# Optimization experiments

Measured on AMD Instinct MI355X. Metric: run time of the kernel, lower is better.

## Reference

```python
import jax, jax.numpy as jnp
import numpy as np

N_NODES = 50000
N_EDGES = 600000
D = 128
R = 8
EPS = 1e-5


def layer_norm(x, g, b):
    mu = jnp.mean(x, axis=-1, keepdims=True)
    var = jnp.mean(jnp.square(x - mu), axis=-1, keepdims=True)
    return (x - mu) * jax.lax.rsqrt(var + EPS) * g + b


def rgcn(x, src, dst, edge_attr, W, root, bias, num_nodes):
    # x: [N, d], W: [R, d, f], edge_attr: [E, R] soft relation weights
    E = src.shape[0]
    f = W.shape[-1]
    msg = jnp.zeros((E, f), dtype=x.dtype)
    for r in range(W.shape[0]):  # small fixed relation count
        hr = x @ W[r]                       # [N, f]
        msg = msg + hr[src] * edge_attr[:, r][:, None]  # gather + weight
    agg = jax.ops.segment_sum(msg, dst, num_segments=num_nodes)  # scatter-add
    return agg + x @ root + bias


def setup_inputs() -> dict:
    key = jax.random.key(0)
    ks = jax.random.split(key, 12)
    s = 1.0 / np.sqrt(D)
    return {
        "x": jax.random.normal(ks[0], (N_NODES, D), dtype=jnp.float32),
        "edge_index": jax.random.randint(ks[1], (2, N_EDGES), 0, N_NODES, dtype=jnp.int64),
        "edge_attr": jax.random.uniform(ks[2], (N_EDGES, R), dtype=jnp.float32),
        "ln1_g": jnp.ones((D,), jnp.float32),
        "ln1_b": jnp.zeros((D,), jnp.float32),
        "W1": jax.random.normal(ks[3], (R, D, D), jnp.float32) * s,
        "root1": jax.random.normal(ks[4], (D, D), jnp.float32) * s,
        "b1": jnp.zeros((D,), jnp.float32),
        "ln2_g": jnp.ones((D,), jnp.float32),
        "ln2_b": jnp.zeros((D,), jnp.float32),
        "W2": jax.random.normal(ks[5], (R, D, D), jnp.float32) * s,
        "root2": jax.random.normal(ks[6], (D, D), jnp.float32) * s,
        "b2": jnp.zeros((D,), jnp.float32),
    }


def reference(x, edge_index, edge_attr, ln1_g, ln1_b, W1, root1, b1,
              ln2_g, ln2_b, W2, root2, b2):
    src, dst = edge_index[0], edge_index[1]
    identity = x
    out = jax.nn.gelu(layer_norm(x, ln1_g, ln1_b), approximate=False)
    out = rgcn(out, src, dst, edge_attr, W1, root1, b1, x.shape[0])
    out = jax.nn.gelu(layer_norm(out, ln2_g, ln2_b), approximate=False)
    out = rgcn(out, src, dst, edge_attr, W2, root2, b2, x.shape[0])
    return out + identity
```

## Files before the change

### kernel.cpp

```cpp
#include <hip/hip_runtime.h>
#include <hip/hip_bf16.h>

typedef __attribute__((ext_vector_type(8))) short short8;
typedef __attribute__((ext_vector_type(4))) float f32x4;

__device__ __forceinline__ float bf2f(unsigned short u) {
    union { unsigned int i; float f; } v; v.i = ((unsigned int)u) << 16; return v.f;
}
__device__ __forceinline__ unsigned short f2bf(float f) {
    __hip_bfloat16 h = __float2bfloat16(f);
    union { __hip_bfloat16 h; unsigned short u; } v; v.h = h; return v.u;
}
__device__ __forceinline__ float gelu_exact(float t) {
    return 0.5f * t * (1.0f + erff(t * 0.70710678118654752f));
}
__device__ __forceinline__ short8 ntload8(const unsigned short* p) {
    return __builtin_nontemporal_load((const short8*)p);
}

__global__ void prep_w(const float* __restrict__ W1, const float* __restrict__ root1,
                       unsigned short* __restrict__ Bf1,
                       const float* __restrict__ W2, const float* __restrict__ root2,
                       unsigned short* __restrict__ Bf2) {
    int i = blockIdx.x * 256 + threadIdx.x;
    const float* W = W1; const float* root = root1; unsigned short* Bfrag = Bf1;
    if (i >= 1152 * 128) {
        i -= 1152 * 128; W = W2; root = root2; Bfrag = Bf2;
        if (i >= 1152 * 128) return;
    }
    int kp = i >> 7, n = i & 127;
    float v;
    if (kp < 1024) {
        int d = kp >> 3, r = kp & 7;
        v = W[((size_t)r * 128 + d) * 128 + n];
    } else {
        v = root[(size_t)(kp - 1024) * 128 + n];
    }
    int kb = kp >> 5;
    int lane = (((kp >> 3) & 3) << 4) | (n & 15);
    int j = kp & 7;
    int t = n >> 4;
    Bfrag[(((size_t)(kb * 8 + t) * 64 + lane) << 3) + j] = f2bf(v);
}

__global__ void zero_i32(int* __restrict__ p, int n) {
    int i = blockIdx.x * 256 + threadIdx.x;
    if (i < n) p[i] = 0;
}

__global__ void hist_dst(const int* __restrict__ ei, int* __restrict__ cnt, int E) {
    int e = blockIdx.x * 256 + threadIdx.x;
    if (e >= E) return;
    atomicAdd(&cnt[ei[E + e]], 1);
}

__global__ void scan1(const int* __restrict__ cnt, int* __restrict__ part,
                      int* __restrict__ bsum, int N) {
    int i = blockIdx.x * 256 + threadIdx.x;
    int v = (i < N) ? cnt[i] : 0;
    int lane = threadIdx.x & 63, wid = threadIdx.x >> 6;
    int s = v;
    #pragma unroll
    for (int off = 1; off < 64; off <<= 1) {
        int t = __shfl_up(s, off);
        if (lane >= off) s += t;
    }
    __shared__ int wsum[4];
    if (lane == 63) wsum[wid] = s;
    __syncthreads();
    int add = 0;
    for (int w = 0; w < wid; ++w) add += wsum[w];
    s += add;
    part[i] = s - v;
    if (threadIdx.x == 255) bsum[blockIdx.x] = s;
}

__global__ void scan2(int* __restrict__ bsum, int nb) {
    int i = threadIdx.x;
    int v = (i < nb) ? bsum[i] : 0;
    int lane = threadIdx.x & 63, wid = threadIdx.x >> 6;
    int s = v;
    #pragma unroll
    for (int off = 1; off < 64; off <<= 1) {
        int t = __shfl_up(s, off);
        if (lane >= off) s += t;
    }
    __shared__ int wsum[4];
    if (lane == 63) wsum[wid] = s;
    __syncthreads();
    int add = 0;
    for (int w = 0; w < wid; ++w) add += wsum[w];
    s += add;
    if (i < nb) bsum[i] = s - v;
}

__global__ void scan3(const int* __restrict__ part, const int* __restrict__ bsum,
                      int* __restrict__ rowptr, int* __restrict__ woff, int N) {
    int i = blockIdx.x * 256 + threadIdx.x;
    if (i >= N) return;
    int v = part[i] + bsum[blockIdx.x];
    rowptr[i] = v;
    woff[i] = v;
}

__global__ void scatter_edges(const int* __restrict__ ei, const float4* __restrict__ attr,
                              int* __restrict__ woff, int* __restrict__ esrc,
                              float4* __restrict__ eattr, int E) {
    int e = blockIdx.x * 256 + threadIdx.x;
    if (e >= E) return;
    int src = ei[e], dst = ei[E + e];
    int p = atomicAdd(&woff[dst], 1);
    esrc[p] = src;
    eattr[2 * p]     = attr[2 * e];
    eattr[2 * p + 1] = attr[2 * e + 1];
}

__global__ void ln_gelu(const float* __restrict__ x, const float* __restrict__ g,
                        const float* __restrict__ b, unsigned short* __restrict__ y, int N) {
    int row = (blockIdx.x * blockDim.x + threadIdx.x) >> 6;
    if (row >= N) return;
    int lane = threadIdx.x & 63;
    size_t off = (size_t)row * 128 + lane * 2;
    float2 v = *(const float2*)(x + off);
    float s = v.x + v.y;
    #pragma unroll
    for (int o = 32; o; o >>= 1) s += __shfl_xor(s, o);
    float mu = s * (1.0f / 128.0f);
    float d0 = v.x - mu, d1 = v.y - mu;
    float q = d0 * d0 + d1 * d1;
    #pragma unroll
    for (int o = 32; o; o >>= 1) q += __shfl_xor(q, o);
    float rs = rsqrtf(q * (1.0f / 128.0f) + 1e-5f);
    float2 gg = *(const float2*)(g + lane * 2);
    float2 bb = *(const float2*)(b + lane * 2);
    ushort2 o2;
    o2.x = f2bf(gelu_exact(d0 * rs * gg.x + bb.x));
    o2.y = f2bf(gelu_exact(d1 * rs * gg.y + bb.y));
    *(ushort2*)(y + off) = o2;
}

__global__ __launch_bounds__(256) void edge_z(const int* __restrict__ rowptr,
                                              const int* __restrict__ esrc,
                                              const float4* __restrict__ eattr,
                                              const unsigned short* __restrict__ y,
                                              unsigned short* __restrict__ z, int N, int E) {
    int row = (blockIdx.x << 2) + (threadIdx.x >> 6);
    if (row >= N) return;
    int lane = threadIdx.x & 63;
    int e0 = rowptr[row];
    int e1 = (row + 1 < N) ? rowptr[row + 1] : E;
    float a0[8] = {0,0,0,0,0,0,0,0};
    float a1[8] = {0,0,0,0,0,0,0,0};

    const unsigned short* yl = y + lane * 2;

    int e = e0;
    for (; e + 4 <= e1; e += 4) {
        int s0 = esrc[e], s1 = esrc[e + 1], s2 = esrc[e + 2], s3 = esrc[e + 3];
        float4 wA0 = eattr[2 * e],     wA1 = eattr[2 * e + 1];
        float4 wB0 = eattr[2 * e + 2], wB1 = eattr[2 * e + 3];
        float4 wC0 = eattr[2 * e + 4], wC1 = eattr[2 * e + 5];
        float4 wD0 = eattr[2 * e + 6], wD1 = eattr[2 * e + 7];
        unsigned int h0 = *(const unsigned int*)(yl + (size_t)s0 * 128);
        unsigned int h1 = *(const unsigned int*)(yl + (size_t)s1 * 128);
        unsigned int h2 = *(const unsigned int*)(yl + (size_t)s2 * 128);
        unsigned int h3 = *(const unsigned int*)(yl + (size_t)s3 * 128);
        float y00 = bf2f((unsigned short)(h0 & 0xffffu)), y01 = bf2f((unsigned short)(h0 >> 16));
        float y10 = bf2f((unsigned short)(h1 & 0xffffu)), y11 = bf2f((unsigned short)(h1 >> 16));
        float y20 = bf2f((unsigned short)(h2 & 0xffffu)), y21 = bf2f((unsigned short)(h2 >> 16));
        float y30 = bf2f((unsigned short)(h3 & 0xffffu)), y31 = bf2f((unsigned short)(h3 >> 16));
        a0[0] += wA0.x * y00; a1[0] += wA0.x * y01;
        a0[1] += wA0.y * y00; a1[1] += wA0.y * y01;
        a0[2] += wA0.z * y00; a1[2] += wA0.z * y01;
        a0[3] += wA0.w * y00; a1[3] += wA0.w * y01;
        a0[4] += wA1.x * y00; a1[4] += wA1.x * y01;
        a0[5] += wA1.y * y00; a1[5] += wA1.y * y01;
        a0[6] += wA1.z * y00; a1[6] += wA1.z * y01;
        a0[7] += wA1.w * y00; a1[7] += wA1.w * y01;
        a0[0] += wB0.x * y10; a1[0] += wB0.x * y11;
        a0[1] += wB0.y * y10; a1[1] += wB0.y * y11;
        a0[2] += wB0.z * y10; a1[2] += wB0.z * y11;
        a0[3] += wB0.w * y10; a1[3] += wB0.w * y11;
        a0[4] += wB1.x * y10; a1[4] += wB1.x * y11;
        a0[5] += wB1.y * y10; a1[5] += wB1.y * y11;
        a0[6] += wB1.z * y10; a1[6] += wB1.z * y11;
        a0[7] += wB1.w * y10; a1[7] += wB1.w * y11;
        a0[0] += wC0.x * y20; a1[0] += wC0.x * y21;
        a0[1] += wC0.y * y20; a1[1] += wC0.y * y21;
        a0[2] += wC0.z * y20; a1[2] += wC0.z * y21;
        a0[3] += wC0.w * y20; a1[3] += wC0.w * y21;
        a0[4] += wC1.x * y20; a1[4] += wC1.x * y21;
        a0[5] += wC1.y * y20; a1[5] += wC1.y * y21;
        a0[6] += wC1.z * y20; a1[6] += wC1.z * y21;
        a0[7] += wC1.w * y20; a1[7] += wC1.w * y21;
        a0[0] += wD0.x * y30; a1[0] += wD0.x * y31;
        a0[1] += wD0.y * y30; a1[1] += wD0.y * y31;
        a0[2] += wD0.z * y30; a1[2] += wD0.z * y31;
        a0[3] += wD0.w * y30; a1[3] += wD0.w * y31;
        a0[4] += wD1.x * y30; a1[4] += wD1.x * y31;
        a0[5] += wD1.y * y30; a1[5] += wD1.y * y31;
        a0[6] += wD1.z * y30; a1[6] += wD1.z * y31;
        a0[7] += wD1.w * y30; a1[7] += wD1.w * y31;
    }
    for (; e < e1; ++e) {
        int src = esrc[e];
        float4 w0 = eattr[2 * e], w1 = eattr[2 * e + 1];
        unsigned int h = *(const unsigned int*)(yl + (size_t)src * 128);
        float y0 = bf2f((unsigned short)(h & 0xffffu)), y1 = bf2f((unsigned short)(h >> 16));
        a0[0] += w0.x * y0; a1[0] += w0.x * y1;
        a0[1] += w0.y * y0; a1[1] += w0.y * y1;
        a0[2] += w0.z * y0; a1[2] += w0.z * y1;
        a0[3] += w0.w * y0; a1[3] += w0.w * y1;
        a0[4] += w1.x * y0; a1[4] += w1.x * y1;
        a0[5] += w1.y * y0; a1[5] += w1.y * y1;
        a0[6] += w1.z * y0; a1[6] += w1.z * y1;
        a0[7] += w1.w * y0; a1[7] += w1.w * y1;
    }
    short8 p0, p1;
    #pragma unroll
    for (int r = 0; r < 8; ++r) {
        p0[r] = (short)f2bf(a0[r]);
        p1[r] = (short)f2bf(a1[r]);
    }
    unsigned short* zr = z + (size_t)row * 1024 + lane * 16;
    __builtin_nontemporal_store(p0, (short8*)zr);
    __builtin_nontemporal_store(p1, (short8*)(zr + 8));
}

template <int MODE>
__global__ __launch_bounds__(256) void gemm_fused(
        const unsigned short* __restrict__ z, const unsigned short* __restrict__ y,
        const unsigned short* __restrict__ Bfrag, const float* __restrict__ bias,
        const float* __restrict__ lng, const float* __restrict__ lnb,
        const float* __restrict__ xres, void* __restrict__ outp, int N) {
    __shared__ short8 Bs[2][512];

    int w = threadIdx.x >> 6;
    int lane = threadIdx.x & 63;
    int l15 = lane & 15, lhi = lane >> 4;
    int m0 = blockIdx.x * 128 + w * 32;

    const unsigned short* za0 = z + (size_t)(m0 + l15) * 1024 + lhi * 8;
    const unsigned short* za1 = za0 + (size_t)16 * 1024;
    const unsigned short* ya0 = y + (size_t)(m0 + l15) * 128 + lhi * 8;
    const unsigned short* ya1 = ya0 + 16 * 128;
    const short8* bfb = (const short8*)Bfrag;

    #define STAGE(buf, kb)                                                         \
        do {                                                                       \
            const short8* gsrc = bfb + (kb) * 512 + w * 128;                       \
            __builtin_amdgcn_global_load_lds(&gsrc[lane],      &Bs[buf][w * 128],      16, 0, 0); \
            __builtin_amdgcn_global_load_lds(&gsrc[64 + lane], &Bs[buf][w * 128 + 64], 16, 0, 0); \
        } while (0)

    STAGE(0, 0);
    short8 a0 = ntload8(za0);
    short8 a1 = ntload8(za1);
    __syncthreads();

    f32x4 acc0[8] = {}, acc1[8] = {};
    for (int kb = 0; kb < 36; ++kb) {
        int cur = kb & 1;
        short8 n0, n1;
        if (kb + 1 < 36) {
            STAGE(cur ^ 1, kb + 1);
            if (kb + 1 < 32) {
                n0 = ntload8(za0 + (kb + 1) * 32);
                n1 = ntload8(za1 + (kb + 1) * 32);
            } else {
                n0 = ntload8(ya0 + (kb + 1 - 32) * 32);
                n1 = ntload8(ya1 + (kb + 1 - 32) * 32);
            }
        }
        #pragma unroll
        for (int t = 0; t < 8; ++t) {
            short8 b = Bs[cur][t * 64 + lane];
            acc0[t] = __builtin_amdgcn_mfma_f32_16x16x32_bf16(a0, b, acc0[t], 0, 0, 0);
            acc1[t] = __builtin_amdgcn_mfma_f32_16x16x32_bf16(a1, b, acc1[t], 0, 0, 0);
        }
        __syncthreads();
        a0 = n0; a1 = n1;
    }
    #undef STAGE

    float bcol[8];
    #pragma unroll
    for (int t = 0; t < 8; ++t) bcol[t] = bias[t * 16 + l15];

    if (MODE == 0) {
        float gcol[8], lbcol[8];
        #pragma unroll
        for (int t = 0; t < 8; ++t) { gcol[t] = lng[t * 16 + l15]; lbcol[t] = lnb[t * 16 + l15]; }
        unsigned short* out = (unsigned short*)outp;
        #pragma unroll
        for (int g = 0; g < 2; ++g) {
            int mb = m0 + g * 16;
            #pragma unroll
            for (int reg = 0; reg < 4; ++reg) {
                int row = mb + lhi * 4 + reg;
                float tv[8];
                float s = 0.f;
                #pragma unroll
                for (int t = 0; t < 8; ++t) {
                    tv[t] = (g ? acc1[t][reg] : acc0[t][reg]) + bcol[t];
                    s += tv[t];
                }
                #pragma unroll
                for (int msk = 1; msk < 16; msk <<= 1) s += __shfl_xor(s, msk);
                float mu = s * (1.0f / 128.0f);
                float q = 0.f;
                #pragma unroll
                for (int t = 0; t < 8; ++t) { float d = tv[t] - mu; q += d * d; }
                #pragma unroll
                for (int msk = 1; msk < 16; msk <<= 1) q += __shfl_xor(q, msk);
                float rs = rsqrtf(q * (1.0f / 128.0f) + 1e-5f);
                if (row < N) {
                    #pragma unroll
                    for (int t = 0; t < 8; ++t) {
                        float u = gelu_exact((tv[t] - mu) * rs * gcol[t] + lbcol[t]);
                        out[(size_t)row * 128 + t * 16 + l15] = f2bf(u);
                    }
                }
            }
        }
    } else {
        float* out = (float*)outp;
        #pragma unroll
        for (int g = 0; g < 2; ++g) {
            int mb = m0 + g * 16;
            #pragma unroll
            for (int reg = 0; reg < 4; ++reg) {
                int row = mb + lhi * 4 + reg;
                if (row < N) {
                    #pragma unroll
                    for (int t = 0; t < 8; ++t) {
                        size_t idx = (size_t)row * 128 + t * 16 + l15;
                        out[idx] = (g ? acc1[t][reg] : acc0[t][reg]) + bcol[t] + xres[idx];
                    }
                }
            }
        }
    }
}

extern "C" void kernel_launch(void* const* d_in, const int* in_sizes, int n_in,
                              void* d_out, int out_size, void* d_ws, size_t ws_size,
                              hipStream_t stream) {
    const float* x     = (const float*)d_in[0];
    const int*   ei    = (const int*)d_in[1];
    const float* attr  = (const float*)d_in[2];
    const float* ln1g  = (const float*)d_in[3];
    const float* ln1b  = (const float*)d_in[4];
    const float* W1    = (const float*)d_in[5];
    const float* root1 = (const float*)d_in[6];
    const float* b1    = (const float*)d_in[7];
    const float* ln2g  = (const float*)d_in[8];
    const float* ln2b  = (const float*)d_in[9];
    const float* W2    = (const float*)d_in[10];
    const float* root2 = (const float*)d_in[11];
    const float* b2    = (const float*)d_in[12];

    const int N = in_sizes[0] / 128;
    const int E = in_sizes[1] / 2;

    char* ws = (char*)d_ws;
    unsigned short* y1    = (unsigned short*)(ws);
    unsigned short* y2    = (unsigned short*)(ws + 12900000);
    unsigned short* z     = (unsigned short*)(ws + 25800000);
    unsigned short* Bf1   = (unsigned short*)(ws + 128400000);
    unsigned short* Bf2   = (unsigned short*)(ws + 128700000);
    int*            cnt   = (int*)(ws + 129000000);
    int*            part  = (int*)(ws + 129210000);
    int*            bsum  = (int*)(ws + 129420000);
    int*            rowptr= (int*)(ws + 129430000);
    int*            woff  = (int*)(ws + 129640000);
    int*            esrc  = (int*)(ws + 129850000);
    float4*         eattr = (float4*)(ws + 132250000);

    const int scanBlocks  = (N + 255) / 256;
    const int edgeBlocksE = (E + 255) / 256;
    const int rowsBlocks  = (N * 64 + 255) / 256;
    const int nodeBlocks  = (N + 3) / 4;
    const int gemmBlocks  = (N + 127) / 128;

    prep_w<<<1152, 256, 0, stream>>>(W1, root1, Bf1, W2, root2, Bf2);

    zero_i32<<<scanBlocks, 256, 0, stream>>>(cnt, scanBlocks * 256);
    hist_dst<<<edgeBlocksE, 256, 0, stream>>>(ei, cnt, E);
    scan1<<<scanBlocks, 256, 0, stream>>>(cnt, part, bsum, N);
    scan2<<<1, 256, 0, stream>>>(bsum, scanBlocks);
    scan3<<<scanBlocks, 256, 0, stream>>>(part, bsum, rowptr, woff, N);
    scatter_edges<<<edgeBlocksE, 256, 0, stream>>>(ei, (const float4*)attr, woff, esrc, eattr, E);

    ln_gelu<<<rowsBlocks, 256, 0, stream>>>(x, ln1g, ln1b, y1, N);
    edge_z<<<nodeBlocks, 256, 0, stream>>>(rowptr, esrc, eattr, y1, z, N, E);
    gemm_fused<0><<<gemmBlocks, 256, 0, stream>>>(z, y1, Bf1, b1, ln2g, ln2b, nullptr, (void*)y2, N);

    edge_z<<<nodeBlocks, 256, 0, stream>>>(rowptr, esrc, eattr, y2, z, N, E);
    gemm_fused<1><<<gemmBlocks, 256, 0, stream>>>(z, y2, Bf2, b2, nullptr, nullptr, x, d_out, N);
}
```

Baseline: 302.3 us.

## Interleave z and y in one row-major A buffer; drop LDS staging in GEMM

Stores the edge aggregates (z) and the LayerNorm/GELU activations (y) side by side in a single buffer with a 1152-element row stride. The GEMM can then walk one contiguous K range per row, and the layer-1 epilogue writes y2 in place. The GEMM no longer stages the weight fragments through LDS with block barriers; each wave double-buffers its B fragments in registers, loaded straight from global/L2. The edge gather is unrolled to 8 independent loads, and the nontemporal loads and stores are removed. The trade-offs are 4x redundant L2 reads of B across waves, higher register pressure, and gathers of y now spread over a larger, strided footprint.

```diff
diff --git a/kernel.cpp b/kernel.cpp
--- a/kernel.cpp
+++ b/kernel.cpp
@@ -3,6 +3,8 @@
 
 typedef __attribute__((ext_vector_type(8))) short short8;
 typedef __attribute__((ext_vector_type(4))) float f32x4;
+
+#define LDA 1152
 
 __device__ __forceinline__ float bf2f(unsigned short u) {
     union { unsigned int i; float f; } v; v.i = ((unsigned int)u) << 16; return v.f;
@@ -13,9 +15,6 @@
 }
 __device__ __forceinline__ float gelu_exact(float t) {
     return 0.5f * t * (1.0f + erff(t * 0.70710678118654752f));
-}
-__device__ __forceinline__ short8 ntload8(const unsigned short* p) {
-    return __builtin_nontemporal_load((const short8*)p);
 }
 
 __global__ void prep_w(const float* __restrict__ W1, const float* __restrict__ root1,
@@ -116,12 +115,11 @@
 }
 
 __global__ void ln_gelu(const float* __restrict__ x, const float* __restrict__ g,
-                        const float* __restrict__ b, unsigned short* __restrict__ y, int N) {
+                        const float* __restrict__ b, unsigned short* __restrict__ A, int N) {
     int row = (blockIdx.x * blockDim.x + threadIdx.x) >> 6;
     if (row >= N) return;
     int lane = threadIdx.x & 63;
-    size_t off = (size_t)row * 128 + lane * 2;
-    float2 v = *(const float2*)(x + off);
+    float2 v = *(const float2*)(x + (size_t)row * 128 + lane * 2);
     float s = v.x + v.y;
     #pragma unroll
     for (int o = 32; o; o >>= 1) s += __shfl_xor(s, o);
@@ -136,14 +134,13 @@
     ushort2 o2;
     o2.x = f2bf(gelu_exact(d0 * rs * gg.x + bb.x));
     o2.y = f2bf(gelu_exact(d1 * rs * gg.y + bb.y));
-    *(ushort2*)(y + off) = o2;
+    *(ushort2*)(A + (size_t)row * LDA + 1024 + lane * 2) = o2;
 }
 
 __global__ __launch_bounds__(256) void edge_z(const int* __restrict__ rowptr,
                                               const int* __restrict__ esrc,
                                               const float4* __restrict__ eattr,
-                                              const unsigned short* __restrict__ y,
-                                              unsigned short* __restrict__ z, int N, int E) {
+                                              unsigned short* __restrict__ A, int N, int E) {
     int row = (blockIdx.x << 2) + (threadIdx.x >> 6);
     if (row >= N) return;
     int lane = threadIdx.x & 63;
@@ -151,137 +148,103 @@
     int e1 = (row + 1 < N) ? rowptr[row + 1] : E;
     float a0[8] = {0,0,0,0,0,0,0,0};
     float a1[8] = {0,0,0,0,0,0,0,0};
-
-    const unsigned short* yl = y + lane * 2;
+    const unsigned short* yl = A + 1024 + lane * 2;
+
+    #define EDGE_FMA(hv, W0, W1) do {                                  \
+        float y0 = bf2f((unsigned short)((hv) & 0xffffu));             \
+        float y1 = bf2f((unsigned short)((hv) >> 16));                 \
+        a0[0] += (W0).x * y0; a1[0] += (W0).x * y1;                    \
+        a0[1] += (W0).y * y0; a1[1] += (W0).y * y1;                    \
+        a0[2] += (W0).z * y0; a1[2] += (W0).z * y1;                    \
+        a0[3] += (W0).w * y0; a1[3] += (W0).w * y1;                    \
+        a0[4] += (W1).x * y0; a1[4] += (W1).x * y1;                    \
+        a0[5] += (W1).y * y0; a1[5] += (W1).y * y1;                    \
+        a0[6] += (W1).z * y0; a1[6] += (W1).z * y1;                    \
+        a0[7] += (W1).w * y0; a1[7] += (W1).w * y1;                    \
+    } while (0)
 
     int e = e0;
+    for (; e + 8 <= e1; e += 8) {
+        unsigned int h[8];
+        #pragma unroll
+        for (int u = 0; u < 8; ++u)
+            h[u] = *(const unsigned int*)(yl + (size_t)esrc[e + u] * LDA);
+        #pragma unroll
+        for (int u = 0; u < 8; ++u) {
+            float4 w0 = eattr[2 * (e + u)], w1 = eattr[2 * (e + u) + 1];
+            EDGE_FMA(h[u], w0, w1);
+        }
+    }
     for (; e + 4 <= e1; e += 4) {
-        int s0 = esrc[e], s1 = esrc[e + 1], s2 = esrc[e + 2], s3 = esrc[e + 3];
-        float4 wA0 = eattr[2 * e],     wA1 = eattr[2 * e + 1];
-        float4 wB0 = eattr[2 * e + 2], wB1 = eattr[2 * e + 3];
-        float4 wC0 = eattr[2 * e + 4], wC1 = eattr[2 * e + 5];
-        float4 wD0 = eattr[2 * e + 6], wD1 = eattr[2 * e + 7];
-        unsigned int h0 = *(const unsigned int*)(yl + (size_t)s0 * 128);
-        unsigned int h1 = *(const unsigned int*)(yl + (size_t)s1 * 128);
-        unsigned int h2 = *(const unsigned int*)(yl + (size_t)s2 * 128);
-        unsigned int h3 = *(const unsigned int*)(yl + (size_t)s3 * 128);
-        float y00 = bf2f((unsigned short)(h0 & 0xffffu)), y01 = bf2f((unsigned short)(h0 >> 16));
-        float y10 = bf2f((unsigned short)(h1 & 0xffffu)), y11 = bf2f((unsigned short)(h1 >> 16));
-        float y20 = bf2f((unsigned short)(h2 & 0xffffu)), y21 = bf2f((unsigned short)(h2 >> 16));
-        float y30 = bf2f((unsigned short)(h3 & 0xffffu)), y31 = bf2f((unsigned short)(h3 >> 16));
-        a0[0] += wA0.x * y00; a1[0] += wA0.x * y01;
-        a0[1] += wA0.y * y00; a1[1] += wA0.y * y01;
-        a0[2] += wA0.z * y00; a1[2] += wA0.z * y01;
-        a0[3] += wA0.w * y00; a1[3] += wA0.w * y01;
-        a0[4] += wA1.x * y00; a1[4] += wA1.x * y01;
-        a0[5] += wA1.y * y00; a1[5] += wA1.y * y01;
-        a0[6] += wA1.z * y00; a1[6] += wA1.z * y01;
-        a0[7] += wA1.w * y00; a1[7] += wA1.w * y01;
-        a0[0] += wB0.x * y10; a1[0] += wB0.x * y11;
-        a0[1] += wB0.y * y10; a1[1] += wB0.y * y11;
-        a0[2] += wB0.z * y10; a1[2] += wB0.z * y11;
-        a0[3] += wB0.w * y10; a1[3] += wB0.w * y11;
-        a0[4] += wB1.x * y10; a1[4] += wB1.x * y11;
-        a0[5] += wB1.y * y10; a1[5] += wB1.y * y11;
-        a0[6] += wB1.z * y10; a1[6] += wB1.z * y11;
-        a0[7] += wB1.w * y10; a1[7] += wB1.w * y11;
-        a0[0] += wC0.x * y20; a1[0] += wC0.x * y21;
-        a0[1] += wC0.y * y20; a1[1] += wC0.y * y21;
-        a0[2] += wC0.z * y20; a1[2] += wC0.z * y21;
-        a0[3] += wC0.w * y20; a1[3] += wC0.w * y21;
-        a0[4] += wC1.x * y20; a1[4] += wC1.x * y21;
-        a0[5] += wC1.y * y20; a1[5] += wC1.y * y21;
-        a0[6] += wC1.z * y20; a1[6] += wC1.z * y21;
-        a0[7] += wC1.w * y20; a1[7] += wC1.w * y21;
-        a0[0] += wD0.x * y30; a1[0] += wD0.x * y31;
-        a0[1] += wD0.y * y30; a1[1] += wD0.y * y31;
-        a0[2] += wD0.z * y30; a1[2] += wD0.z * y31;
-        a0[3] += wD0.w * y30; a1[3] += wD0.w * y31;
-        a0[4] += wD1.x * y30; a1[4] += wD1.x * y31;
-        a0[5] += wD1.y * y30; a1[5] += wD1.y * y31;
-        a0[6] += wD1.z * y30; a1[6] += wD1.z * y31;
-        a0[7] += wD1.w * y30; a1[7] += wD1.w * y31;
+        unsigned int h[4];
+        #pragma unroll
+        for (int u = 0; u < 4; ++u)
+            h[u] = *(const unsigned int*)(yl + (size_t)esrc[e + u] * LDA);
+        #pragma unroll
+        for (int u = 0; u < 4; ++u) {
+            float4 w0 = eattr[2 * (e + u)], w1 = eattr[2 * (e + u) + 1];
+            EDGE_FMA(h[u], w0, w1);
+        }
     }
     for (; e < e1; ++e) {
-        int src = esrc[e];
+        unsigned int h = *(const unsigned int*)(yl + (size_t)esrc[e] * LDA);
         float4 w0 = eattr[2 * e], w1 = eattr[2 * e + 1];
-        unsigned int h = *(const unsigned int*)(yl + (size_t)src * 128);
-        float y0 = bf2f((unsigned short)(h & 0xffffu)), y1 = bf2f((unsigned short)(h >> 16));
-        a0[0] += w0.x * y0; a1[0] += w0.x * y1;
-        a0[1] += w0.y * y0; a1[1] += w0.y * y1;
-        a0[2] += w0.z * y0; a1[2] += w0.z * y1;
-        a0[3] += w0.w * y0; a1[3] += w0.w * y1;
-        a0[4] += w1.x * y0; a1[4] += w1.x * y1;
-        a0[5] += w1.y * y0; a1[5] += w1.y * y1;
-        a0[6] += w1.z * y0; a1[6] += w1.z * y1;
-        a0[7] += w1.w * y0; a1[7] += w1.w * y1;
-    }
+        EDGE_FMA(h, w0, w1);
+    }
+    #undef EDGE_FMA
+
     short8 p0, p1;
     #pragma unroll
-    for (int r = 0; r < 8; ++r) {
-        p0[r] = (short)f2bf(a0[r]);
-        p1[r] = (short)f2bf(a1[r]);
-    }
-    unsigned short* zr = z + (size_t)row * 1024 + lane * 16;
-    __builtin_nontemporal_store(p0, (short8*)zr);
-    __builtin_nontemporal_store(p1, (short8*)(zr + 8));
+    for (int r = 0; r < 8; ++r) { p0[r] = (short)f2bf(a0[r]); p1[r] = (short)f2bf(a1[r]); }
+    unsigned short* zr = A + (size_t)row * LDA + lane * 16;
+    *(short8*)zr = p0;
+    *(short8*)(zr + 8) = p1;
 }
 
 template <int MODE>
 __global__ __launch_bounds__(256) void gemm_fused(
-        const unsigned short* __restrict__ z, const unsigned short* __restrict__ y,
-        const unsigned short* __restrict__ Bfrag, const float* __restrict__ bias,
-        const float* __restrict__ lng, const float* __restrict__ lnb,
-        const float* __restrict__ xres, void* __restrict__ outp, int N) {
-    __shared__ short8 Bs[2][512];
-
-    int w = threadIdx.x >> 6;
+        unsigned short* __restrict__ A, const unsigned short* __restrict__ Bfrag,
+        const float* __restrict__ bias, const float* __restrict__ lng,
+        const float* __restrict__ lnb, const float* __restrict__ xres,
+        float* __restrict__ outp, int N) {
+    int gw = (blockIdx.x * 256 + threadIdx.x) >> 6;
     int lane = threadIdx.x & 63;
     int l15 = lane & 15, lhi = lane >> 4;
-    int m0 = blockIdx.x * 128 + w * 32;
-
-    const unsigned short* za0 = z + (size_t)(m0 + l15) * 1024 + lhi * 8;
-    const unsigned short* za1 = za0 + (size_t)16 * 1024;
-    const unsigned short* ya0 = y + (size_t)(m0 + l15) * 128 + lhi * 8;
-    const unsigned short* ya1 = ya0 + 16 * 128;
-    const short8* bfb = (const short8*)Bfrag;
-
-    #define STAGE(buf, kb)                                                         \
-        do {                                                                       \
-            const short8* gsrc = bfb + (kb) * 512 + w * 128;                       \
-            __builtin_amdgcn_global_load_lds(&gsrc[lane],      &Bs[buf][w * 128],      16, 0, 0); \
-            __builtin_amdgcn_global_load_lds(&gsrc[64 + lane], &Bs[buf][w * 128 + 64], 16, 0, 0); \
-        } while (0)
-
-    STAGE(0, 0);
-    short8 a0 = ntload8(za0);
-    short8 a1 = ntload8(za1);
-    __syncthreads();
+    int m0 = gw * 32;
+
+    const unsigned short* a0p = A + (size_t)(m0 + l15) * LDA + lhi * 8;
+    const unsigned short* a1p = a0p + 16 * LDA;
+    const short8* bfb = (const short8*)Bfrag + lane;
+
+    short8 bA[8], bB[8];
+    #pragma unroll
+    for (int t = 0; t < 8; ++t) bA[t] = bfb[t * 64];
+    short8 aA0 = *(const short8*)a0p;
+    short8 aA1 = *(const short8*)a1p;
 
     f32x4 acc0[8] = {}, acc1[8] = {};
-    for (int kb = 0; kb < 36; ++kb) {
-        int cur = kb & 1;
-        short8 n0, n1;
-        if (kb + 1 < 36) {
-            STAGE(cur ^ 1, kb + 1);
-            if (kb + 1 < 32) {
-                n0 = ntload8(za0 + (kb + 1) * 32);
-                n1 = ntload8(za1 + (kb + 1) * 32);
-            } else {
-                n0 = ntload8(ya0 + (kb + 1 - 32) * 32);
-                n1 = ntload8(ya1 + (kb + 1 - 32) * 32);
-            }
-        }
+    for (int kb = 0; kb < 36; kb += 2) {
+        #pragma unroll
+        for (int t = 0; t < 8; ++t) bB[t] = bfb[((kb + 1) * 8 + t) * 64];
+        short8 aB0 = *(const short8*)(a0p + (kb + 1) * 32);
+        short8 aB1 = *(const short8*)(a1p + (kb + 1) * 32);
         #pragma unroll
         for (int t = 0; t < 8; ++t) {
-            short8 b = Bs[cur][t * 64 + lane];
-            acc0[t] = __builtin_amdgcn_mfma_f32_16x16x32_bf16(a0, b, acc0[t], 0, 0, 0);
-            acc1[t] = __builtin_amdgcn_mfma_f32_16x16x32_bf16(a1, b, acc1[t], 0, 0, 0);
-        }
-        __syncthreads();
-        a0 = n0; a1 = n1;
-    }
-    #undef STAGE
+            acc0[t] = __builtin_amdgcn_mfma_f32_16x16x32_bf16(aA0, bA[t], acc0[t], 0, 0, 0);
+            acc1[t] = __builtin_amdgcn_mfma_f32_16x16x32_bf16(aA1, bA[t], acc1[t], 0, 0, 0);
+        }
+        if (kb + 2 < 36) {
+            #pragma unroll
+            for (int t = 0; t < 8; ++t) bA[t] = bfb[((kb + 2) * 8 + t) * 64];
+            aA0 = *(const short8*)(a0p + (kb + 2) * 32);
+            aA1 = *(const short8*)(a1p + (kb + 2) * 32);
+        }
+        #pragma unroll
+        for (int t = 0; t < 8; ++t) {
+            acc0[t] = __builtin_amdgcn_mfma_f32_16x16x32_bf16(aB0, bB[t], acc0[t], 0, 0, 0);
+            acc1[t] = __builtin_amdgcn_mfma_f32_16x16x32_bf16(aB1, bB[t], acc1[t], 0, 0, 0);
+        }
+    }
 
     float bcol[8];
     #pragma unroll
@@ -291,7 +254,6 @@
         float gcol[8], lbcol[8];
         #pragma unroll
         for (int t = 0; t < 8; ++t) { gcol[t] = lng[t * 16 + l15]; lbcol[t] = lnb[t * 16 + l15]; }
-        unsigned short* out = (unsigned short*)outp;
         #pragma unroll
         for (int g = 0; g < 2; ++g) {
             int mb = m0 + g * 16;
@@ -318,13 +280,12 @@
                     #pragma unroll
                     for (int t = 0; t < 8; ++t) {
                         float u = gelu_exact((tv[t] - mu) * rs * gcol[t] + lbcol[t]);
-                        out[(size_t)row * 128 + t * 16 + l15] = f2bf(u);
+                        A[(size_t)row * LDA + 1024 + t * 16 + l15] = f2bf(u);
                     }
                 }
             }
         }
     } else {
-        float* out = (float*)outp;
         #pragma unroll
         for (int g = 0; g < 2; ++g) {
             int mb = m0 + g * 16;
@@ -335,7 +296,7 @@
                     #pragma unroll
                     for (int t = 0; t < 8; ++t) {
                         size_t idx = (size_t)row * 128 + t * 16 + l15;
-                        out[idx] = (g ? acc1[t][reg] : acc0[t][reg]) + bcol[t] + xres[idx];
+                        outp[idx] = (g ? acc1[t][reg] : acc0[t][reg]) + bcol[t] + xres[idx];
                     }
                 }
             }
@@ -364,18 +325,16 @@
     const int E = in_sizes[1] / 2;
 
     char* ws = (char*)d_ws;
-    unsigned short* y1    = (unsigned short*)(ws);
-    unsigned short* y2    = (unsigned short*)(ws + 12900000);
-    unsigned short* z     = (unsigned short*)(ws + 25800000);
-    unsigned short* Bf1   = (unsigned short*)(ws + 128400000);
-    unsigned short* Bf2   = (unsigned short*)(ws + 128700000);
-    int*            cnt   = (int*)(ws + 129000000);
-    int*            part  = (int*)(ws + 129210000);
-    int*            bsum  = (int*)(ws + 129420000);
-    int*            rowptr= (int*)(ws + 129430000);
-    int*            woff  = (int*)(ws + 129640000);
-    int*            esrc  = (int*)(ws + 129850000);
-    float4*         eattr = (float4*)(ws + 132250000);
+    unsigned short* A     = (unsigned short*)(ws);
+    unsigned short* Bf1   = (unsigned short*)(ws + 115400000);
+    unsigned short* Bf2   = (unsigned short*)(ws + 115700000);
+    int*            cnt   = (int*)(ws + 116000000);
+    int*            part  = (int*)(ws + 116210000);
+    int*            bsum  = (int*)(ws + 116420000);
+    int*            rowptr= (int*)(ws + 116430000);
+    int*            woff  = (int*)(ws + 116640000);
+    int*            esrc  = (int*)(ws + 116850000);
+    float4*         eattr = (float4*)(ws + 119250000);
 
     const int scanBlocks  = (N + 255) / 256;
     const int edgeBlocksE = (E + 255) / 256;
@@ -392,10 +351,10 @@
     scan3<<<scanBlocks, 256, 0, stream>>>(part, bsum, rowptr, woff, N);
     scatter_edges<<<edgeBlocksE, 256, 0, stream>>>(ei, (const float4*)attr, woff, esrc, eattr, E);
 
-    ln_gelu<<<rowsBlocks, 256, 0, stream>>>(x, ln1g, ln1b, y1, N);
-    edge_z<<<nodeBlocks, 256, 0, stream>>>(rowptr, esrc, eattr, y1, z, N, E);
-    gemm_fused<0><<<gemmBlocks, 256, 0, stream>>>(z, y1, Bf1, b1, ln2g, ln2b, nullptr, (void*)y2, N);
-
-    edge_z<<<nodeBlocks, 256, 0, stream>>>(rowptr, esrc, eattr, y2, z, N, E);
-    gemm_fused<1><<<gemmBlocks, 256, 0, stream>>>(z, y2, Bf2, b2, nullptr, nullptr, x, d_out, N);
-}
+    ln_gelu<<<rowsBlocks, 256, 0, stream>>>(x, ln1g, ln1b, A, N);
+    edge_z<<<nodeBlocks, 256, 0, stream>>>(rowptr, esrc, eattr, A, N, E);
+    gemm_fused<0><<<gemmBlocks, 256, 0, stream>>>(A, Bf1, b1, ln2g, ln2b, nullptr, nullptr, N);
+
+    edge_z<<<nodeBlocks, 256, 0, stream>>>(rowptr, esrc, eattr, A, N, E);
+    gemm_fused<1><<<gemmBlocks, 256, 0, stream>>>(A, Bf2, b2, nullptr, nullptr, x, (float*)d_out, N);
+}
```

Measured after the change: 302.2 us. About the same (-0.0%).
